# Performance work log

Measured on AMD Instinct MI355X. Metric: run time of the kernel, lower is better.

The kernel has to match this reference:

```python
import jax, jax.numpy as jnp
import numpy as np

NUM_HEADS = 16
HEAD_DIM = 64
NEG_INF = -1000000000.0


def rotary_embedding(x, seq_len, head_dim):
    # x: (batch, seq, heads, head_dim)
    positions = jnp.arange(seq_len)
    dim_pairs = jnp.arange(0, head_dim, 2)
    freqs = 1.0 / 10000.0 ** (dim_pairs / head_dim)
    angles = positions[:, None] * freqs[None, :]          # (seq, head_dim/2)
    cos = jnp.cos(angles)[:, None, :]                     # (seq, 1, head_dim/2) -> broadcast over heads
    sin = jnp.sin(angles)[:, None, :]
    x1 = x[..., ::2]
    x2 = x[..., 1::2]
    out1 = x1 * cos - x2 * sin
    out2 = x1 * sin + x2 * cos
    return jnp.stack([out1, out2], axis=-1).reshape(x.shape)


def setup_inputs() -> dict:
    key = jax.random.key(0)
    k1, k2, k3 = jax.random.split(key, 3)
    batch, seq_len, embed_dim = 2, 2048, 1024
    x = jax.random.normal(k1, (batch, seq_len, embed_dim), dtype=jnp.float32)
    W_qkv = jax.random.normal(k2, (embed_dim, 3 * NUM_HEADS * HEAD_DIM), dtype=jnp.float32) * 0.02
    W_out = jax.random.normal(k3, (NUM_HEADS * HEAD_DIM, embed_dim), dtype=jnp.float32) * 0.02
    return {"x": x, "W_qkv": W_qkv, "W_out": W_out}


def reference(x, W_qkv, W_out):
    batch, seq_len, embed_dim = x.shape
    qkv = jnp.einsum('bse,ef->bsf', x, W_qkv)
    qkv = qkv.reshape(batch, seq_len, 3, NUM_HEADS, HEAD_DIM)
    q, k, v = qkv[:, :, 0], qkv[:, :, 1], qkv[:, :, 2]
    q = rotary_embedding(q, seq_len, HEAD_DIM)
    k = rotary_embedding(k, seq_len, HEAD_DIM)
    scale = 1.0 / jnp.sqrt(jnp.asarray(HEAD_DIM, dtype=x.dtype))
    scores = jnp.einsum('bqhd,bkhd->bhqk', q, k) * scale   # (B,H,S,S)
    mask = jnp.tril(jnp.ones((seq_len, seq_len), dtype=bool))[None, None, :, :]
    scores = jnp.where(mask, scores, NEG_INF)
    weights = jax.nn.softmax(scores, axis=-1)
    out = jnp.einsum('bhqk,bkhd->bqhd', weights, v)
    out = out.reshape(batch, seq_len, NUM_HEADS * HEAD_DIM)
    return jnp.einsum('bsf,fe->bse', out, W_out)
```

## Files before the change

kernel.cpp:

```cpp
#include <hip/hip_runtime.h>
#include <hip/hip_bf16.h>

typedef __attribute__((ext_vector_type(8))) short short8;
typedef __attribute__((ext_vector_type(4))) float float4v;

__global__ __launch_bounds__(256) void prep_all(
    const float* __restrict__ x, __hip_bfloat16* __restrict__ xb,
    float2* __restrict__ tab,
    const float* __restrict__ Wqkv, const float* __restrict__ Wout,
    __hip_bfloat16* __restrict__ WqkvT, __hip_bfloat16* __restrict__ WoutT) {
  __shared__ __hip_bfloat16 tile[32][33];
  const int id = blockIdx.x;
  if (id < 4096) {
    const int i = id * 256 + threadIdx.x;
    const float4 v = *(const float4*)(x + (size_t)i * 4);
    __hip_bfloat16 o[4];
    o[0] = __float2bfloat16(v.x); o[1] = __float2bfloat16(v.y);
    o[2] = __float2bfloat16(v.z); o[3] = __float2bfloat16(v.w);
    *(uint2*)(xb + (size_t)i * 4) = *(const uint2*)o;
    return;
  }
  if (id < 4352) {
    const int i = (id - 4096) * 256 + threadIdx.x;
    const int s = i >> 5, p = i & 31;
    const float freq = powf(10000.f, -(float)(p * 2) / 64.f);
    float sn, cs;
    sincosf((float)s * freq, &sn, &cs);
    tab[i] = make_float2(cs, sn);
    return;
  }
  const float* in;
  __hip_bfloat16* out;
  int C, bx, by;
  if (id < 7424) {
    const int lid = id - 4352;
    in = Wqkv; out = WqkvT; C = 3072; bx = lid % 96; by = lid / 96;
  } else {
    const int lid = id - 7424;
    in = Wout; out = WoutT; C = 1024; bx = lid & 31; by = lid >> 5;
  }
  const int R = 1024;
  const int c0 = bx * 32, r0 = by * 32;
  const int tx = threadIdx.x & 31, ty = threadIdx.x >> 5;
  #pragma unroll
  for (int i = ty; i < 32; i += 8)
    tile[i][tx] = __float2bfloat16(in[(size_t)(r0 + i) * C + (c0 + tx)]);
  __syncthreads();
  #pragma unroll
  for (int i = ty; i < 32; i += 8)
    out[(size_t)(c0 + i) * R + (r0 + tx)] = tile[tx][i];
}

template <typename OutT, int BM, int BN>
__global__ __launch_bounds__(256) void gemm_bt(
    const __hip_bfloat16* __restrict__ A,
    const __hip_bfloat16* __restrict__ Bt,
    OutT* __restrict__ C,
    int M, int N, int K) {
  __shared__ __hip_bfloat16 lA[BM][64];
  __shared__ __hip_bfloat16 lB[BN][64];
  constexpr int NI = BM / 32, NJ = BN / 32;
  const int t = threadIdx.x;
  const int lane = t & 63, wave = t >> 6;
  const int quad = lane >> 4, ln = lane & 15;
  const int m0 = blockIdx.y * BM, n0 = blockIdx.x * BN;
  const int wm = (wave >> 1) * (BM / 2), wn = (wave & 1) * (BN / 2);
  const int srow = lane >> 3;
  const int schunk = ((lane & 7) ^ srow) * 8;

  float4v acc[NI][NJ];
  #pragma unroll
  for (int i = 0; i < NI; ++i)
    #pragma unroll
    for (int j = 0; j < NJ; ++j)
      acc[i][j] = (float4v){0.f, 0.f, 0.f, 0.f};

  for (int kt = 0; kt < K; kt += 64) {
    __syncthreads();
    #pragma unroll
    for (int g = 0; g < BM / 32; ++g) {
      const int rbase = wave * (BM / 4) + g * 8;
      __builtin_amdgcn_global_load_lds(
          (const __attribute__((address_space(1))) void*)
              (A + (size_t)(m0 + rbase + srow) * K + kt + schunk),
          (__attribute__((address_space(3))) void*)&lA[rbase][0], 16, 0, 0);
    }
    #pragma unroll
    for (int g = 0; g < BN / 32; ++g) {
      const int rbase = wave * (BN / 4) + g * 8;
      __builtin_amdgcn_global_load_lds(
          (const __attribute__((address_space(1))) void*)
              (Bt + (size_t)(n0 + rbase + srow) * K + kt + schunk),
          (__attribute__((address_space(3))) void*)&lB[rbase][0], 16, 0, 0);
    }
    __syncthreads();
    #pragma unroll
    for (int step = 0; step < 2; ++step) {
      short8 af[NI], bf[NJ];
      #pragma unroll
      for (int i = 0; i < NI; ++i)
        af[i] = *(const short8*)&lA[wm + i * 16 + ln][((step * 4 + quad) ^ (ln & 7)) * 8];
      #pragma unroll
      for (int j = 0; j < NJ; ++j)
        bf[j] = *(const short8*)&lB[wn + j * 16 + ln][((step * 4 + quad) ^ (ln & 7)) * 8];
      #pragma unroll
      for (int i = 0; i < NI; ++i)
        #pragma unroll
        for (int j = 0; j < NJ; ++j)
          acc[i][j] = __builtin_amdgcn_mfma_f32_16x16x32_bf16(af[i], bf[j], acc[i][j], 0, 0, 0);
    }
  }
  #pragma unroll
  for (int i = 0; i < NI; ++i)
    #pragma unroll
    for (int j = 0; j < NJ; ++j)
      #pragma unroll
      for (int r = 0; r < 4; ++r) {
        const int row = m0 + wm + i * 16 + quad * 4 + r;
        const int col = n0 + wn + j * 16 + ln;
        if constexpr (__is_same(OutT, float))
          C[(size_t)row * N + col] = acc[i][j][r];
        else
          C[(size_t)row * N + col] = __float2bfloat16(acc[i][j][r]);
      }
}

__global__ __launch_bounds__(256) void qkv_prep(
    const __hip_bfloat16* __restrict__ qkv,
    const float2* __restrict__ tab,
    __hip_bfloat16* __restrict__ Q,
    __hip_bfloat16* __restrict__ K,
    __hip_bfloat16* __restrict__ Vt) {
  __shared__ __hip_bfloat16 tile[64][65];
  const int s0 = blockIdx.x * 64;
  const int bh = blockIdx.y;
  const int h = bh & 15, b = bh >> 4;
  const int t = threadIdx.x;

  const int pr = t & 31, sl = t >> 5;
  const int d0 = pr * 2;
  const float qs = 0.125f * 1.44269504088896340736f;
  #pragma unroll
  for (int ss = sl; ss < 64; ss += 8) {
    const int s = s0 + ss;
    const float2 cssn = tab[(size_t)s * 32 + pr];
    const float cs = cssn.x, sn = cssn.y;
    const size_t in_base = (size_t)(b * 2048 + s) * 3072;
    const size_t o = ((size_t)bh * 2048 + s) * 64 + d0;

    __hip_bfloat162 q2 = *(const __hip_bfloat162*)&qkv[in_base + h * 64 + d0];
    float x1 = __bfloat162float(q2.x), x2 = __bfloat162float(q2.y);
    __hip_bfloat162 qo;
    qo.x = __float2bfloat16((x1 * cs - x2 * sn) * qs);
    qo.y = __float2bfloat16((x1 * sn + x2 * cs) * qs);
    *(__hip_bfloat162*)&Q[o] = qo;

    __hip_bfloat162 k2 = *(const __hip_bfloat162*)&qkv[in_base + 1024 + h * 64 + d0];
    x1 = __bfloat162float(k2.x); x2 = __bfloat162float(k2.y);
    __hip_bfloat162 ko;
    ko.x = __float2bfloat16(x1 * cs - x2 * sn);
    ko.y = __float2bfloat16(x1 * sn + x2 * cs);
    *(__hip_bfloat162*)&K[o] = ko;
  }

  const int tx = t & 63, ty = t >> 6;
  #pragma unroll
  for (int i = ty; i < 64; i += 4)
    tile[i][tx] = qkv[(size_t)(b * 2048 + s0 + i) * 3072 + 2048 + h * 64 + tx];
  __syncthreads();
  #pragma unroll
  for (int i = ty; i < 64; i += 4)
    Vt[((size_t)bh * 64 + i) * 2048 + s0 + tx] = tile[tx][i];
}

__global__ __launch_bounds__(256) void attention(
    const __hip_bfloat16* __restrict__ Q,
    const __hip_bfloat16* __restrict__ K,
    const __hip_bfloat16* __restrict__ Vt,
    __hip_bfloat16* __restrict__ attn) {
  __shared__ __hip_bfloat16 lK[2][64][64];
  __shared__ __hip_bfloat16 lV[2][64][64];
  __shared__ __hip_bfloat16 lO[4][16][64];
  const int t = threadIdx.x;
  const int lane = t & 63, w = t >> 6;
  const int quad = lane >> 4, ln = lane & 15;
  const int id = blockIdx.x;
  const int bh = id & 31;
  const int j = id >> 5;
  const int k2 = j >> 3, g = j & 7;
  const int qt = 8 * k2 + ((k2 & 1) ? (7 - g) : g);
  const int q0 = qt * 64;
  const size_t base = (size_t)bh * 2048 * 64;
  const __hip_bfloat16* Qb = Q + base;
  const __hip_bfloat16* Kb = K + base;
  const __hip_bfloat16* Vb = Vt + base;
  const int b = bh >> 4, h = bh & 15;

  const int srow = lane >> 3;
  const int schunk = ((lane & 7) ^ srow) * 8;
  const int rb0 = w * 16;
  const int sig_base = (ln >> 2) * 8 + (ln & 3);

  #pragma unroll
  for (int g2 = 0; g2 < 2; ++g2) {
    const int rbase = rb0 + g2 * 8;
    __builtin_amdgcn_global_load_lds(
        (const __attribute__((address_space(1))) void*)
            (Kb + (size_t)(rbase + srow) * 64 + schunk),
        (__attribute__((address_space(3))) void*)&lK[0][rbase][0], 16, 0, 0);
    __builtin_amdgcn_global_load_lds(
        (const __attribute__((address_space(1))) void*)
            (Vb + (size_t)(rbase + srow) * 2048 + schunk),
        (__attribute__((address_space(3))) void*)&lV[0][rbase][0], 16, 0, 0);
  }

  short8 qf[2];
  {
    const size_t qrow = (size_t)(q0 + w * 16 + ln) * 64;
    qf[0] = *(const short8*)(Qb + qrow + quad * 8);
    qf[1] = *(const short8*)(Qb + qrow + 32 + quad * 8);
  }

  float4v acc_o[4];
  #pragma unroll
  for (int dt = 0; dt < 4; ++dt) acc_o[dt] = (float4v){0.f, 0.f, 0.f, 0.f};
  float suml = 0.f;

  for (int kt = 0; kt <= qt; ++kt) {
    const int buf = kt & 1;
    __syncthreads();

    if (kt < qt) {
      #pragma unroll
      for (int g2 = 0; g2 < 2; ++g2) {
        const int rbase = rb0 + g2 * 8;
        __builtin_amdgcn_global_load_lds(
            (const __attribute__((address_space(1))) void*)
                (Kb + (size_t)((kt + 1) * 64 + rbase + srow) * 64 + schunk),
            (__attribute__((address_space(3))) void*)&lK[buf ^ 1][rbase][0], 16, 0, 0);
        __builtin_amdgcn_global_load_lds(
            (const __attribute__((address_space(1))) void*)
                (Vb + (size_t)(rbase + srow) * 2048 + (kt + 1) * 64 + schunk),
            (__attribute__((address_space(3))) void*)&lV[buf ^ 1][rbase][0], 16, 0, 0);
      }
    }

    float4v s4[4];
    #pragma unroll
    for (int nt = 0; nt < 4; ++nt) {
      const int krow = sig_base + ((nt & 1) << 2) + ((nt >> 1) << 5);
      const int k7 = krow & 7;
      float4v a = (float4v){0.f, 0.f, 0.f, 0.f};
      #pragma unroll
      for (int step = 0; step < 2; ++step) {
        short8 kf = *(const short8*)&lK[buf][krow][((step * 4 + quad) ^ k7) * 8];
        a = __builtin_amdgcn_mfma_f32_16x16x32_bf16(kf, qf[step], a, 0, 0, 0);
      }
      s4[nt] = a;
    }
    if (kt == qt) {
      const int qr = q0 + w * 16 + ln;
      #pragma unroll
      for (int nt = 0; nt < 4; ++nt)
        #pragma unroll
        for (int r = 0; r < 4; ++r) {
          const int kglob = kt * 64 + quad * 8 + ((nt & 1) << 2) + r + ((nt >> 1) << 5);
          if (kglob > qr) s4[nt][r] = -64.f;
        }
    }
    #pragma unroll
    for (int nt = 0; nt < 4; ++nt)
      #pragma unroll
      for (int r = 0; r < 4; ++r) {
        s4[nt][r] = __builtin_amdgcn_exp2f(s4[nt][r]);
        suml += s4[nt][r];
      }
    #pragma unroll
    for (int s = 0; s < 2; ++s) {
      union { short8 v; short e[8]; } pb;
      #pragma unroll
      for (int i = 0; i < 4; ++i) {
        __hip_bfloat16 b0 = __float2bfloat16(s4[2 * s][i]);
        __hip_bfloat16 b1 = __float2bfloat16(s4[2 * s + 1][i]);
        pb.e[i] = *reinterpret_cast<short*>(&b0);
        pb.e[4 + i] = *reinterpret_cast<short*>(&b1);
      }
      #pragma unroll
      for (int dt = 0; dt < 4; ++dt) {
        short8 vf = *(const short8*)&lV[buf][dt * 16 + ln][((s * 4 + quad) ^ (ln & 7)) * 8];
        acc_o[dt] = __builtin_amdgcn_mfma_f32_16x16x32_bf16(vf, pb.v, acc_o[dt], 0, 0, 0);
      }
    }
  }

  float l0 = suml + __shfl_xor(suml, 16);
  const float inv = 1.0f / (l0 + __shfl_xor(l0, 32));

  #pragma unroll
  for (int dt = 0; dt < 4; ++dt)
    #pragma unroll
    for (int r = 0; r < 4; ++r)
      lO[w][ln][dt * 16 + quad * 4 + r] = __float2bfloat16(acc_o[dt][r] * inv);

  const int orow = lane >> 2;
  const int od = (lane & 3) * 16;
  const uint4 w0 = *(const uint4*)&lO[w][orow][od];
  const uint4 w1 = *(const uint4*)&lO[w][orow][od + 8];
  const size_t rg = (size_t)(b * 2048 + q0 + w * 16 + orow);
  *(uint4*)&attn[rg * 1024 + h * 64 + od] = w0;
  *(uint4*)&attn[rg * 1024 + h * 64 + od + 8] = w1;
}

extern "C" void kernel_launch(void* const* d_in, const int* in_sizes, int n_in,
                              void* d_out, int out_size, void* d_ws, size_t ws_size,
                              hipStream_t stream) {
  const float* x    = (const float*)d_in[0];
  const float* Wqkv = (const float*)d_in[1];
  const float* Wout = (const float*)d_in[2];
  float* out = (float*)d_out;

  __hip_bfloat16* ws = (__hip_bfloat16*)d_ws;
  __hip_bfloat16* xb    = ws;
  __hip_bfloat16* WqkvT = xb    + (size_t)4096 * 1024;
  __hip_bfloat16* WoutT = WqkvT + (size_t)3072 * 1024;
  __hip_bfloat16* qkv   = WoutT + (size_t)1024 * 1024;
  __hip_bfloat16* Q     = qkv   + (size_t)4096 * 3072;
  __hip_bfloat16* K     = Q     + (size_t)32 * 2048 * 64;
  __hip_bfloat16* Vt    = K     + (size_t)32 * 2048 * 64;
  __hip_bfloat16* attn  = Vt    + (size_t)32 * 2048 * 64;
  float2*         tab   = (float2*)(attn + (size_t)4096 * 1024);

  prep_all<<<8448, 256, 0, stream>>>(x, xb, tab, Wqkv, Wout, WqkvT, WoutT);
  gemm_bt<__hip_bfloat16, 128, 128><<<dim3(3072 / 128, 4096 / 128), 256, 0, stream>>>(xb, WqkvT, qkv, 4096, 3072, 1024);
  qkv_prep<<<dim3(32, 32), 256, 0, stream>>>(qkv, tab, Q, K, Vt);
  attention<<<1024, 256, 0, stream>>>(Q, K, Vt, attn);
  gemm_bt<float, 128, 64><<<dim3(1024 / 64, 4096 / 128), 256, 0, stream>>>(attn, WoutT, out, 4096, 1024, 1024);
}
```

Measured before the change: 177.9 us.

## Replace QKV GEMM with 256x256 tile, 4-stage global_load_lds pipelined kernel

```diff
diff --git a/kernel.cpp b/kernel.cpp
--- a/kernel.cpp
+++ b/kernel.cpp
@@ -122,6 +122,101 @@
           C[(size_t)row * N + col] = acc[i][j][r];
         else
           C[(size_t)row * N + col] = __float2bfloat16(acc[i][j][r]);
+      }
+}
+
+__global__ __launch_bounds__(512, 2) void gemm1_pipe(
+    const __hip_bfloat16* __restrict__ A,
+    const __hip_bfloat16* __restrict__ Bt,
+    __hip_bfloat16* __restrict__ C) {
+  constexpr int KD = 1024, NN = 3072, NT = KD / 32;
+  __shared__ __hip_bfloat16 lA[4][256][32];
+  __shared__ __hip_bfloat16 lB[4][256][32];
+  const int t = threadIdx.x;
+  const int lane = t & 63, w = t >> 6;
+  const int quad = lane >> 4, ln = lane & 15;
+  const int m0 = blockIdx.y * 256, n0 = blockIdx.x * 256;
+  const int wm = (w >> 2) * 128, wn = (w & 3) * 64;
+  const int srow = t >> 2;
+  const int dch  = t & 3;
+  const int gch  = dch ^ ((t >> 3) & 3);
+  const int rch = (quad ^ ((ln >> 1) & 3)) * 8;
+
+  float4v acc[8][4];
+  #pragma unroll
+  for (int mq = 0; mq < 8; ++mq)
+    #pragma unroll
+    for (int nq = 0; nq < 4; ++nq)
+      acc[mq][nq] = (float4v){0.f, 0.f, 0.f, 0.f};
+
+  auto STAGE = [&](int tile) {
+    const int buf = tile & 3;
+    #pragma unroll
+    for (int g = 0; g < 2; ++g) {
+      const int row = g * 128 + srow;
+      __builtin_amdgcn_global_load_lds(
+          (const __attribute__((address_space(1))) void*)
+              (A + (size_t)(m0 + row) * KD + tile * 32 + gch * 8),
+          (__attribute__((address_space(3))) void*)&lA[buf][row][dch * 8], 16, 0, 0);
+    }
+    #pragma unroll
+    for (int g = 0; g < 2; ++g) {
+      const int row = g * 128 + srow;
+      __builtin_amdgcn_global_load_lds(
+          (const __attribute__((address_space(1))) void*)
+              (Bt + (size_t)(n0 + row) * KD + tile * 32 + gch * 8),
+          (__attribute__((address_space(3))) void*)&lB[buf][row][dch * 8], 16, 0, 0);
+    }
+  };
+
+  auto COMPUTE = [&](int tile) {
+    const int buf = tile & 3;
+    short8 af[8], bf[4];
+    #pragma unroll
+    for (int mq = 0; mq < 8; ++mq)
+      af[mq] = *(const short8*)&lA[buf][wm + mq * 16 + ln][rch];
+    #pragma unroll
+    for (int nq = 0; nq < 4; ++nq)
+      bf[nq] = *(const short8*)&lB[buf][wn + nq * 16 + ln][rch];
+    __builtin_amdgcn_s_setprio(1);
+    #pragma unroll
+    for (int mq = 0; mq < 8; ++mq)
+      #pragma unroll
+      for (int nq = 0; nq < 4; ++nq)
+        acc[mq][nq] = __builtin_amdgcn_mfma_f32_16x16x32_bf16(af[mq], bf[nq], acc[mq][nq], 0, 0, 0);
+    __builtin_amdgcn_s_setprio(0);
+  };
+
+  STAGE(0); STAGE(1); STAGE(2);
+
+  for (int tile = 0; tile < NT - 2; ++tile) {
+    asm volatile("s_waitcnt vmcnt(8)" ::: "memory");
+    __builtin_amdgcn_sched_barrier(0);
+    __builtin_amdgcn_s_barrier();
+    __builtin_amdgcn_sched_barrier(0);
+    if (tile < NT - 3) STAGE(tile + 3);
+    COMPUTE(tile);
+  }
+  asm volatile("s_waitcnt vmcnt(4)" ::: "memory");
+  __builtin_amdgcn_sched_barrier(0);
+  __builtin_amdgcn_s_barrier();
+  __builtin_amdgcn_sched_barrier(0);
+  COMPUTE(NT - 2);
+  asm volatile("s_waitcnt vmcnt(0)" ::: "memory");
+  __builtin_amdgcn_sched_barrier(0);
+  __builtin_amdgcn_s_barrier();
+  __builtin_amdgcn_sched_barrier(0);
+  COMPUTE(NT - 1);
+
+  #pragma unroll
+  for (int mq = 0; mq < 8; ++mq)
+    #pragma unroll
+    for (int nq = 0; nq < 4; ++nq)
+      #pragma unroll
+      for (int r = 0; r < 4; ++r) {
+        const int row = m0 + wm + mq * 16 + quad * 4 + r;
+        const int col = n0 + wn + nq * 16 + ln;
+        C[(size_t)row * NN + col] = __float2bfloat16(acc[mq][nq][r]);
       }
 }
 
@@ -331,7 +426,7 @@
   float2*         tab   = (float2*)(attn + (size_t)4096 * 1024);
 
   prep_all<<<8448, 256, 0, stream>>>(x, xb, tab, Wqkv, Wout, WqkvT, WoutT);
-  gemm_bt<__hip_bfloat16, 128, 128><<<dim3(3072 / 128, 4096 / 128), 256, 0, stream>>>(xb, WqkvT, qkv, 4096, 3072, 1024);
+  gemm1_pipe<<<dim3(3072 / 256, 4096 / 256), 512, 0, stream>>>(xb, WqkvT, qkv);
   qkv_prep<<<dim3(32, 32), 256, 0, stream>>>(qkv, tab, Q, K, Vt);
   attention<<<1024, 256, 0, stream>>>(Q, K, Vt, attn);
   gemm_bt<float, 128, 64><<<dim3(1024 / 64, 4096 / 128), 256, 0, stream>>>(attn, WoutT, out, 4096, 1024, 1024);
```

New measurement: 185.0 us. +4.0%, slower.

## Use 128-row query tiles with 8 waves sharing each K/V tile in attention

Applied to the files above, without the earlier changes.

```diff
diff --git a/kernel.cpp b/kernel.cpp
--- a/kernel.cpp
+++ b/kernel.cpp
@@ -173,23 +173,24 @@
     Vt[((size_t)bh * 64 + i) * 2048 + s0 + tx] = tile[tx][i];
 }
 
-__global__ __launch_bounds__(256) void attention(
+__global__ __launch_bounds__(512) void attention(
     const __hip_bfloat16* __restrict__ Q,
     const __hip_bfloat16* __restrict__ K,
     const __hip_bfloat16* __restrict__ Vt,
     __hip_bfloat16* __restrict__ attn) {
   __shared__ __hip_bfloat16 lK[2][64][64];
   __shared__ __hip_bfloat16 lV[2][64][64];
-  __shared__ __hip_bfloat16 lO[4][16][64];
+  __shared__ __hip_bfloat16 lO[8][16][64];
   const int t = threadIdx.x;
   const int lane = t & 63, w = t >> 6;
   const int quad = lane >> 4, ln = lane & 15;
   const int id = blockIdx.x;
   const int bh = id & 31;
-  const int j = id >> 5;
-  const int k2 = j >> 3, g = j & 7;
-  const int qt = 8 * k2 + ((k2 & 1) ? (7 - g) : g);
-  const int q0 = qt * 64;
+  const int v = id >> 5;
+  const int u = (v < 8) ? v : 23 - v;
+  const int q0 = u * 128;
+  const int NT = 2 * u + 2;
+  const int ktmask = 2 * u + (w >> 2);
   const size_t base = (size_t)bh * 2048 * 64;
   const __hip_bfloat16* Qb = Q + base;
   const __hip_bfloat16* Kb = K + base;
@@ -198,21 +199,17 @@
 
   const int srow = lane >> 3;
   const int schunk = ((lane & 7) ^ srow) * 8;
-  const int rb0 = w * 16;
+  const int krow_st = w * 8 + srow;
   const int sig_base = (ln >> 2) * 8 + (ln & 3);
 
-  #pragma unroll
-  for (int g2 = 0; g2 < 2; ++g2) {
-    const int rbase = rb0 + g2 * 8;
-    __builtin_amdgcn_global_load_lds(
-        (const __attribute__((address_space(1))) void*)
-            (Kb + (size_t)(rbase + srow) * 64 + schunk),
-        (__attribute__((address_space(3))) void*)&lK[0][rbase][0], 16, 0, 0);
-    __builtin_amdgcn_global_load_lds(
-        (const __attribute__((address_space(1))) void*)
-            (Vb + (size_t)(rbase + srow) * 2048 + schunk),
-        (__attribute__((address_space(3))) void*)&lV[0][rbase][0], 16, 0, 0);
-  }
+  __builtin_amdgcn_global_load_lds(
+      (const __attribute__((address_space(1))) void*)
+          (Kb + (size_t)krow_st * 64 + schunk),
+      (__attribute__((address_space(3))) void*)&lK[0][krow_st & 63][0], 16, 0, 0);
+  __builtin_amdgcn_global_load_lds(
+      (const __attribute__((address_space(1))) void*)
+          (Vb + (size_t)krow_st * 2048 + schunk),
+      (__attribute__((address_space(3))) void*)&lV[0][krow_st & 63][0], 16, 0, 0);
 
   short8 qf[2];
   {
@@ -226,69 +223,67 @@
   for (int dt = 0; dt < 4; ++dt) acc_o[dt] = (float4v){0.f, 0.f, 0.f, 0.f};
   float suml = 0.f;
 
-  for (int kt = 0; kt <= qt; ++kt) {
+  for (int kt = 0; kt < NT; ++kt) {
     const int buf = kt & 1;
     __syncthreads();
 
-    if (kt < qt) {
-      #pragma unroll
-      for (int g2 = 0; g2 < 2; ++g2) {
-        const int rbase = rb0 + g2 * 8;
-        __builtin_amdgcn_global_load_lds(
-            (const __attribute__((address_space(1))) void*)
-                (Kb + (size_t)((kt + 1) * 64 + rbase + srow) * 64 + schunk),
-            (__attribute__((address_space(3))) void*)&lK[buf ^ 1][rbase][0], 16, 0, 0);
-        __builtin_amdgcn_global_load_lds(
-            (const __attribute__((address_space(1))) void*)
-                (Vb + (size_t)(rbase + srow) * 2048 + (kt + 1) * 64 + schunk),
-            (__attribute__((address_space(3))) void*)&lV[buf ^ 1][rbase][0], 16, 0, 0);
+    if (kt + 1 < NT) {
+      __builtin_amdgcn_global_load_lds(
+          (const __attribute__((address_space(1))) void*)
+              (Kb + (size_t)((kt + 1) * 64 + krow_st) * 64 + schunk),
+          (__attribute__((address_space(3))) void*)&lK[buf ^ 1][krow_st][0], 16, 0, 0);
+      __builtin_amdgcn_global_load_lds(
+          (const __attribute__((address_space(1))) void*)
+              (Vb + (size_t)krow_st * 2048 + (kt + 1) * 64 + schunk),
+          (__attribute__((address_space(3))) void*)&lV[buf ^ 1][krow_st][0], 16, 0, 0);
+    }
+
+    if (kt <= ktmask) {
+      float4v s4[4];
+      #pragma unroll
+      for (int nt = 0; nt < 4; ++nt) {
+        const int krow = sig_base + ((nt & 1) << 2) + ((nt >> 1) << 5);
+        const int k7 = krow & 7;
+        float4v a = (float4v){0.f, 0.f, 0.f, 0.f};
+        #pragma unroll
+        for (int step = 0; step < 2; ++step) {
+          short8 kf = *(const short8*)&lK[buf][krow][((step * 4 + quad) ^ k7) * 8];
+          a = __builtin_amdgcn_mfma_f32_16x16x32_bf16(kf, qf[step], a, 0, 0, 0);
+        }
+        s4[nt] = a;
       }
-    }
-
-    float4v s4[4];
-    #pragma unroll
-    for (int nt = 0; nt < 4; ++nt) {
-      const int krow = sig_base + ((nt & 1) << 2) + ((nt >> 1) << 5);
-      const int k7 = krow & 7;
-      float4v a = (float4v){0.f, 0.f, 0.f, 0.f};
-      #pragma unroll
-      for (int step = 0; step < 2; ++step) {
-        short8 kf = *(const short8*)&lK[buf][krow][((step * 4 + quad) ^ k7) * 8];
-        a = __builtin_amdgcn_mfma_f32_16x16x32_bf16(kf, qf[step], a, 0, 0, 0);
+      if (kt == ktmask) {
+        const int qr = q0 + w * 16 + ln;
+        #pragma unroll
+        for (int nt = 0; nt < 4; ++nt)
+          #pragma unroll
+          for (int r = 0; r < 4; ++r) {
+            const int kglob = kt * 64 + quad * 8 + ((nt & 1) << 2) + r + ((nt >> 1) << 5);
+            if (kglob > qr) s4[nt][r] = -64.f;
+          }
       }
-      s4[nt] = a;
-    }
-    if (kt == qt) {
-      const int qr = q0 + w * 16 + ln;
       #pragma unroll
       for (int nt = 0; nt < 4; ++nt)
         #pragma unroll
         for (int r = 0; r < 4; ++r) {
-          const int kglob = kt * 64 + quad * 8 + ((nt & 1) << 2) + r + ((nt >> 1) << 5);
-          if (kglob > qr) s4[nt][r] = -64.f;
+          s4[nt][r] = __builtin_amdgcn_exp2f(s4[nt][r]);
+          suml += s4[nt][r];
         }
-    }
-    #pragma unroll
-    for (int nt = 0; nt < 4; ++nt)
-      #pragma unroll
-      for (int r = 0; r < 4; ++r) {
-        s4[nt][r] = __builtin_amdgcn_exp2f(s4[nt][r]);
-        suml += s4[nt][r];
-      }
-    #pragma unroll
-    for (int s = 0; s < 2; ++s) {
-      union { short8 v; short e[8]; } pb;
-      #pragma unroll
-      for (int i = 0; i < 4; ++i) {
-        __hip_bfloat16 b0 = __float2bfloat16(s4[2 * s][i]);
-        __hip_bfloat16 b1 = __float2bfloat16(s4[2 * s + 1][i]);
-        pb.e[i] = *reinterpret_cast<short*>(&b0);
-        pb.e[4 + i] = *reinterpret_cast<short*>(&b1);
-      }
-      #pragma unroll
-      for (int dt = 0; dt < 4; ++dt) {
-        short8 vf = *(const short8*)&lV[buf][dt * 16 + ln][((s * 4 + quad) ^ (ln & 7)) * 8];
-        acc_o[dt] = __builtin_amdgcn_mfma_f32_16x16x32_bf16(vf, pb.v, acc_o[dt], 0, 0, 0);
+      #pragma unroll
+      for (int s = 0; s < 2; ++s) {
+        union { short8 v; short e[8]; } pb;
+        #pragma unroll
+        for (int i = 0; i < 4; ++i) {
+          __hip_bfloat16 b0 = __float2bfloat16(s4[2 * s][i]);
+          __hip_bfloat16 b1 = __float2bfloat16(s4[2 * s + 1][i]);
+          pb.e[i] = *reinterpret_cast<short*>(&b0);
+          pb.e[4 + i] = *reinterpret_cast<short*>(&b1);
+        }
+        #pragma unroll
+        for (int dt = 0; dt < 4; ++dt) {
+          short8 vf = *(const short8*)&lV[buf][dt * 16 + ln][((s * 4 + quad) ^ (ln & 7)) * 8];
+          acc_o[dt] = __builtin_amdgcn_mfma_f32_16x16x32_bf16(vf, pb.v, acc_o[dt], 0, 0, 0);
+        }
       }
     }
   }
@@ -333,6 +328,6 @@
   prep_all<<<8448, 256, 0, stream>>>(x, xb, tab, Wqkv, Wout, WqkvT, WoutT);
   gemm_bt<__hip_bfloat16, 128, 128><<<dim3(3072 / 128, 4096 / 128), 256, 0, stream>>>(xb, WqkvT, qkv, 4096, 3072, 1024);
   qkv_prep<<<dim3(32, 32), 256, 0, stream>>>(qkv, tab, Q, K, Vt);
-  attention<<<1024, 256, 0, stream>>>(Q, K, Vt, attn);
+  attention<<<512, 512, 0, stream>>>(Q, K, Vt, attn);
   gemm_bt<float, 128, 64><<<dim3(1024 / 64, 4096 / 128), 256, 0, stream>>>(attn, WoutT, out, 4096, 1024, 1024);
 }
```

Result: no change. 180.0 us (+1.2%).
